# Kernel tuning notes

Measured on AMD Instinct MI355X. Metric: run time of the kernel, lower is better.

Reference implementation:

```python
import jax, jax.numpy as jnp
import numpy as np

B, T, E, V = 4096, 200, 64, 100000
A1, A2 = 64, 32        # attention MLP dims
M1, M2 = 256, 128      # final MLP dims


def setup_inputs() -> dict:
    key = jax.random.key(0)
    ks = jax.random.split(key, 16)
    w = lambda k, shp: (jax.random.normal(k, shp, dtype=jnp.float32) * 0.02)
    return {
        "target_item": jax.random.randint(ks[0], (B,), 0, V),
        "hist_item_id": jax.random.randint(ks[1], (B, T), 0, V),
        "hist_item_id_mask": jnp.ones((B, T), dtype=bool),
        "embed_table": w(ks[2], (V, E)),
        # attention MLP: 4E -> A1 -> A2 -> 1
        "aw1": w(ks[3], (4 * E, A1)), "ab1": jnp.zeros((A1,), jnp.float32),
        "aw2": w(ks[4], (A1, A2)),   "ab2": jnp.zeros((A2,), jnp.float32),
        "aow": w(ks[5], (A2, 1)),    "aob": jnp.zeros((1,), jnp.float32),
        # final MLP: 2E -> M1 -> M2 -> 1
        "mw1": w(ks[6], (2 * E, M1)), "mb1": jnp.zeros((M1,), jnp.float32),
        "mw2": w(ks[7], (M1, M2)),    "mb2": jnp.zeros((M2,), jnp.float32),
        "ow": w(ks[8], (M2, 1)),      "ob": jnp.zeros((1,), jnp.float32),
    }


def reference(target_item, hist_item_id, hist_item_id_mask, embed_table,
              aw1, ab1, aw2, ab2, aow, aob, mw1, mb1, mw2, mb2, ow, ob):
    item_emb = embed_table[target_item]          # [B, E]
    hist_emb = embed_table[hist_item_id]         # [B, T, E]
    q = jnp.broadcast_to(item_emb[:, None, :], hist_emb.shape)  # [B, T, E]
    attn_in = jnp.concatenate([hist_emb, q, hist_emb - q, hist_emb * q], axis=-1)  # [B, T, 4E]
    h = jax.nn.relu(jnp.einsum("bti,ij->btj", attn_in, aw1) + ab1)
    h = jax.nn.relu(jnp.einsum("bti,ij->btj", h, aw2) + ab2)
    scores = (jnp.einsum("bti,io->bto", h, aow) + aob)[..., 0]  # [B, T]
    scores = jnp.where(hist_item_id_mask, scores, -1e9)
    weights = jax.nn.softmax(scores, axis=-1)                   # [B, T]
    interest = jnp.einsum("bt,bte->be", weights, hist_emb)      # [B, E]
    mlp_in = jnp.concatenate([item_emb, interest], axis=-1)     # [B, 2E]
    g = jax.nn.relu(mlp_in @ mw1 + mb1)
    g = jax.nn.relu(g @ mw2 + mb2)
    return g @ ow + ob                                          # [B, 1]
```

## Files before the change

### kernel.cpp

```cpp
#include <hip/hip_runtime.h>
#include <stdint.h>

#define Bq 4096
#define Tq 200
#define TP 208
#define NMT 13
#define Vq 100000
#define BPB 8

typedef __attribute__((ext_vector_type(8))) short short8;
typedef __attribute__((ext_vector_type(4))) float f32x4;
typedef __attribute__((ext_vector_type(4))) unsigned short bfx4;
typedef __attribute__((ext_vector_type(4))) unsigned int u32x4;

static __device__ __forceinline__ unsigned short f2b(float f) {
    unsigned int u = __builtin_bit_cast(unsigned int, f);
    u = u + 0x7fffu + ((u >> 16) & 1u);
    return (unsigned short)(u >> 16);
}
static __device__ __forceinline__ float b2f(unsigned short s) {
    unsigned int u = ((unsigned int)s) << 16;
    return __builtin_bit_cast(float, u);
}
static __device__ __forceinline__ unsigned int pack2(float lo, float hi) {
    unsigned int r;
    asm volatile("v_cvt_pk_bf16_f32 %0, %1, %2" : "=v"(r) : "v"(lo), "v"(hi));
    return r;
}

static __device__ __forceinline__ short8 ld8sw(const unsigned short* base, int row, int col8) {
    return *(const short8*)((const char*)base + (((row << 7) + (col8 << 1)) ^ ((row & 7) << 4)));
}
static __device__ __forceinline__ void st16sw(unsigned short* base, int row, int col, unsigned short v) {
    *(unsigned short*)((char*)base + (((row << 7) + (col << 1)) ^ ((row & 7) << 4))) = v;
}
static __device__ __forceinline__ void st64sw(unsigned short* base, int row, int col4, bfx4 v) {
    *(bfx4*)((char*)base + (((row << 7) + (col4 << 3)) ^ ((row & 7) << 4))) = v;
}
static __device__ __forceinline__ void st128sw(unsigned short* base, int row, int col8, short8 v) {
    *(short8*)((char*)base + (((row << 7) + (col8 << 1)) ^ ((row & 7) << 4))) = v;
}

extern "C" __global__ __launch_bounds__(256) void k_weff(
    const int* __restrict__ target, const float* __restrict__ embed,
    const float* __restrict__ aw1, const float* __restrict__ ab1,
    const float* __restrict__ aw2,
    unsigned short* __restrict__ weff_all, float* __restrict__ qc_all,
    unsigned short* __restrict__ aw2t, unsigned short* __restrict__ embf)
{
    __shared__ float s_C[64][64];
    __shared__ float s_W3[64][64];
    __shared__ float s_W12T[64][65];
    __shared__ float s_qb[BPB][64];
    int tid = threadIdx.x;
    int b0 = blockIdx.x * BPB;

    for (int idx = tid; idx < 4096; idx += 256) {
        int i = idx >> 6, j = idx & 63;
        float a0 = aw1[i * 64 + j];
        float a1 = aw1[(64 + i) * 64 + j];
        float a2 = aw1[(128 + i) * 64 + j];
        float a3 = aw1[(192 + i) * 64 + j];
        s_C[i][j] = a0 + a2;
        s_W3[i][j] = a3;
        s_W12T[j][i] = a1 - a2;
    }
    for (int idx = tid; idx < BPB * 64; idx += 256) {
        int bb = idx >> 6, j = idx & 63;
        s_qb[bb][j] = embed[(long)target[b0 + bb] * 64 + j];
    }
    if (blockIdx.x == 0) {
        for (int idx = tid; idx < 2048; idx += 256) {
            int j = idx >> 5, k = idx & 31;
            aw2t[k * 64 + j] = f2b(aw2[j * 32 + k]);
        }
    }
    __syncthreads();

    for (int p = tid; p < BPB * 64; p += 256) {
        int bb = p >> 6, j = p & 63;
        float acc = ab1[j];
        #pragma unroll 8
        for (int i = 0; i < 64; ++i)
            acc += s_qb[bb][i] * s_W12T[j][i];
        qc_all[(long)(b0 + bb) * 64 + j] = acc;
    }
    int jw = tid >> 2, i0 = (tid & 3) << 4;
    for (int bb = 0; bb < BPB; ++bb) {
        unsigned int pk[8];
        #pragma unroll
        for (int u = 0; u < 8; ++u) {
            int i = i0 + u * 2;
            float w0 = s_C[i][jw] + s_qb[bb][i] * s_W3[i][jw];
            float w1 = s_C[i + 1][jw] + s_qb[bb][i + 1] * s_W3[i + 1][jw];
            pk[u] = pack2(w0, w1);
        }
        u32x4* dst = (u32x4*)(weff_all + (((long)(b0 + bb)) << 12) + jw * 64 + i0);
        u32x4 v0 = { pk[0], pk[1], pk[2], pk[3] };
        u32x4 v1 = { pk[4], pk[5], pk[6], pk[7] };
        dst[0] = v0;
        dst[1] = v1;
    }
    if (embf) {
        long gsz = (long)gridDim.x * 256;
        for (long i = (long)blockIdx.x * 256 + tid; i < (long)Vq * 8; i += gsz) {
            const float* src = embed + i * 8;
            f32x4 e0 = *(const f32x4*)src;
            f32x4 e1 = *(const f32x4*)(src + 4);
            u32x4 pk = { pack2(e0.x, e0.y), pack2(e0.z, e0.w),
                         pack2(e1.x, e1.y), pack2(e1.z, e1.w) };
            *(u32x4*)(embf + i * 8) = pk;
        }
    }
}

extern "C" __global__ __launch_bounds__(256, 4) void k_attn_fast(
    const int* __restrict__ hist, const int* __restrict__ mask,
    const float* __restrict__ embed,
    const float* __restrict__ ab2, const float* __restrict__ aow,
    const float* __restrict__ aob,
    const unsigned short* __restrict__ weff_all,
    const float* __restrict__ qc_all,
    const unsigned short* __restrict__ aw2t,
    const unsigned short* __restrict__ embf,
    float* __restrict__ inter64)
{
    __shared__ alignas(16) unsigned short s_hist[TP * 64];
    __shared__ float s_sc[TP];
    __shared__ float s_red[8];
    __shared__ float s_intp[4][64];

    int tid = threadIdx.x;
    int lane = tid & 63;
    int wv = tid >> 6;
    int b = blockIdx.x;
    int r16 = lane & 15;
    int kg = lane >> 4;

    int tt[7];
    short8 g[7];
    #pragma unroll
    for (int k = 0; k < 7; ++k) {
        int u = tid + k * 256;
        int t = u >> 3;
        if (u < TP * 8) {
            int tc = (t < Tq) ? t : 0;
            int id = hist[b * Tq + tc];
            g[k] = *(const short8*)(embf + (long)id * 64 + (u & 7) * 8);
        }
        tt[k] = t;
    }
    int mk = (tid < Tq) ? mask[(long)b * Tq + tid] : 0;

    short8 wf[4][2];
    #pragma unroll
    for (int n = 0; n < 4; ++n)
        #pragma unroll
        for (int h = 0; h < 2; ++h)
            wf[n][h] = *(const short8*)(weff_all + (((long)b) << 12) + (n * 16 + r16) * 64 + h * 32 + kg * 8);
    short8 af[2][2];
    #pragma unroll
    for (int n = 0; n < 2; ++n)
        #pragma unroll
        for (int h = 0; h < 2; ++h)
            af[n][h] = *(const short8*)(aw2t + (n * 16 + r16) * 64 + h * 32 + kg * 8);
    f32x4 qcv[4];
    #pragma unroll
    for (int n = 0; n < 4; ++n)
        qcv[n] = *(const f32x4*)&qc_all[(long)b * 64 + n * 16 + kg * 4];
    f32x4 ab2v[2], aowv[2];
    #pragma unroll
    for (int n = 0; n < 2; ++n) {
        ab2v[n] = *(const f32x4*)&ab2[n * 16 + kg * 4];
        aowv[n] = *(const f32x4*)&aow[n * 16 + kg * 4];
    }
    float aob0 = aob[0];

    #pragma unroll
    for (int k = 0; k < 7; ++k) {
        int u = tid + k * 256;
        if (u < TP * 8) st128sw(s_hist, tt[k], (u & 7) * 8, g[k]);
    }
    __syncthreads();

    int srcA = r16 + (((kg << 1) & 3) << 4);
    int srcB = srcA + 16;

    for (int m = wv; m < NMT; m += 4) {
        int row0 = m * 16;
        short8 a0 = ld8sw(s_hist, row0 + r16, kg * 8);
        short8 a1 = ld8sw(s_hist, row0 + r16, 32 + kg * 8);
        f32x4 d[4];
        #pragma unroll
        for (int n = 0; n < 4; ++n) {
            f32x4 z = qcv[n];
            z = __builtin_amdgcn_mfma_f32_16x16x32_bf16(wf[n][0], a0, z, 0, 0, 0);
            z = __builtin_amdgcn_mfma_f32_16x16x32_bf16(wf[n][1], a1, z, 0, 0, 0);
            d[n] = z;
        }
        unsigned int p0[4], p1[4];
        #pragma unroll
        for (int n = 0; n < 4; ++n) {
            p0[n] = pack2(fmaxf(d[n][0], 0.f), fmaxf(d[n][1], 0.f));
            p1[n] = pack2(fmaxf(d[n][2], 0.f), fmaxf(d[n][3], 0.f));
        }
        u32x4 w0, w1;
        {
            unsigned int xA0 = __shfl(p0[0], srcA), xA1 = __shfl(p0[1], srcA);
            unsigned int yA0 = __shfl(p1[0], srcA), yA1 = __shfl(p1[1], srcA);
            unsigned int xB0 = __shfl(p0[0], srcB), xB1 = __shfl(p0[1], srcB);
            unsigned int yB0 = __shfl(p1[0], srcB), yB1 = __shfl(p1[1], srcB);
            w0.x = (kg < 2) ? xA0 : xA1;
            w0.y = (kg < 2) ? yA0 : yA1;
            w0.z = (kg < 2) ? xB0 : xB1;
            w0.w = (kg < 2) ? yB0 : yB1;
            unsigned int uA0 = __shfl(p0[2], srcA), uA1 = __shfl(p0[3], srcA);
            unsigned int vA0 = __shfl(p1[2], srcA), vA1 = __shfl(p1[3], srcA);
            unsigned int uB0 = __shfl(p0[2], srcB), uB1 = __shfl(p0[3], srcB);
            unsigned int vB0 = __shfl(p1[2], srcB), vB1 = __shfl(p1[3], srcB);
            w1.x = (kg < 2) ? uA0 : uA1;
            w1.y = (kg < 2) ? vA0 : vA1;
            w1.z = (kg < 2) ? uB0 : uB1;
            w1.w = (kg < 2) ? vB0 : vB1;
        }
        short8 bh0 = __builtin_bit_cast(short8, w0);
        short8 bh1 = __builtin_bit_cast(short8, w1);
        f32x4 e[2];
        #pragma unroll
        for (int n = 0; n < 2; ++n) {
            f32x4 z = { 0.f, 0.f, 0.f, 0.f };
            z = __builtin_amdgcn_mfma_f32_16x16x32_bf16(af[n][0], bh0, z, 0, 0, 0);
            z = __builtin_amdgcn_mfma_f32_16x16x32_bf16(af[n][1], bh1, z, 0, 0, 0);
            e[n] = z;
        }
        float sacc = 0.f;
        #pragma unroll
        for (int n = 0; n < 2; ++n)
            #pragma unroll
            for (int r = 0; r < 4; ++r)
                sacc += fmaxf(e[n][r] + ab2v[n][r], 0.f) * aowv[n][r];
        sacc += __shfl_xor(sacc, 16);
        sacc += __shfl_xor(sacc, 32);
        if (kg == 0) s_sc[row0 + r16] = sacc + aob0;
    }
    __syncthreads();

    float sc = (tid < Tq) ? (mk ? s_sc[tid] : -1e9f) : -1e30f;
    float mx = sc;
    #pragma unroll
    for (int off = 1; off < 64; off <<= 1) mx = fmaxf(mx, __shfl_xor(mx, off));
    if (lane == 0) s_red[wv] = mx;
    __syncthreads();
    mx = fmaxf(fmaxf(s_red[0], s_red[1]), fmaxf(s_red[2], s_red[3]));
    float ex = (tid < Tq) ? expf(sc - mx) : 0.f;
    float sm = ex;
    #pragma unroll
    for (int off = 1; off < 64; off <<= 1) sm += __shfl_xor(sm, off);
    if (lane == 0) s_red[4 + wv] = sm;
    __syncthreads();
    float tot = s_red[4] + s_red[5] + s_red[6] + s_red[7];
    if (tid < Tq) s_sc[tid] = ex / tot;
    else if (tid < TP) s_sc[tid] = 0.f;
    __syncthreads();

    int cg = lane & 7;
    int tg = lane >> 3;
    float acc8[8];
    #pragma unroll
    for (int u = 0; u < 8; ++u) acc8[u] = 0.f;
    for (int t = wv * 8 + tg; t < TP; t += 32) {
        float w = s_sc[t];
        short8 h = ld8sw(s_hist, t, cg * 8);
        #pragma unroll
        for (int u = 0; u < 8; ++u) acc8[u] += w * b2f((unsigned short)h[u]);
    }
    #pragma unroll
    for (int u = 0; u < 8; ++u) {
        acc8[u] += __shfl_xor(acc8[u], 8);
        acc8[u] += __shfl_xor(acc8[u], 16);
        acc8[u] += __shfl_xor(acc8[u], 32);
    }
    if (tg == 0) {
        #pragma unroll
        for (int u = 0; u < 8; ++u) s_intp[wv][cg * 8 + u] = acc8[u];
    }
    __syncthreads();
    if (tid < 64)
        inter64[(long)b * 64 + tid] = s_intp[0][tid] + s_intp[1][tid] + s_intp[2][tid] + s_intp[3][tid];
}

extern "C" __global__ __launch_bounds__(256, 3) void k_attn_fb(
    const int* __restrict__ target, const int* __restrict__ hist,
    const int* __restrict__ mask,
    const float* __restrict__ embed, const float* __restrict__ aw1,
    const float* __restrict__ ab1, const float* __restrict__ aw2,
    const float* __restrict__ ab2, const float* __restrict__ aow,
    const float* __restrict__ aob,
    float* __restrict__ inter64)
{
    __shared__ int s_id[TP];
    __shared__ float s_q[64];
    __shared__ float s_qc[64];
    __shared__ float s_qcp[4][64];
    __shared__ alignas(16) unsigned short s_hist[TP * 64];
    __shared__ alignas(16) unsigned short s_WeffT[64 * 64];
    __shared__ alignas(16) unsigned short s_aw2T[32 * 64];
    __shared__ alignas(16) unsigned short s_h1[4 * 16 * 64];
    __shared__ float s_sc[TP];
    __shared__ float s_aow[32];
    __shared__ float s_ab2[32];
    __shared__ float s_red[8];
    __shared__ float s_intp[4][64];

    int tid = threadIdx.x;
    int lane = tid & 63;
    int wv = tid >> 6;
    int b = blockIdx.x;

    int tgt = target[b];
    if (tid < 64) s_q[tid] = embed[(long)tgt * 64 + tid];
    for (int t = tid; t < TP; t += 256) s_id[t] = hist[b * Tq + ((t < Tq) ? t : 0)];
    if (tid < 32) { s_aow[tid] = aow[tid]; s_ab2[tid] = ab2[tid]; }
    __syncthreads();

    for (int idx = tid; idx < 4096; idx += 256) {
        int i = idx >> 6, j = idx & 63;
        float w = aw1[i * 64 + j] + aw1[(128 + i) * 64 + j] + s_q[i] * aw1[(192 + i) * 64 + j];
        st16sw(s_WeffT, j, i, f2b(w));
    }
    for (int idx = tid; idx < 2048; idx += 256) {
        int j = idx >> 5, k = idx & 31;
        st16sw(s_aw2T, k, j, f2b(aw2[j * 32 + k]));
    }
    {
        float acc = 0.f;
        #pragma unroll
        for (int ii = 0; ii < 16; ++ii) {
            int i = wv * 16 + ii;
            acc += s_q[i] * (aw1[(64 + i) * 64 + lane] - aw1[(128 + i) * 64 + lane]);
        }
        s_qcp[wv][lane] = acc;
    }
    for (int u = tid; u < TP * 16; u += 256) {
        int t = u >> 4, j4 = u & 15;
        f32x4 e = *(const f32x4*)&embed[(long)s_id[t] * 64 + j4 * 4];
        bfx4 p = { f2b(e.x), f2b(e.y), f2b(e.z), f2b(e.w) };
        st64sw(s_hist, t, j4, p);
    }
    __syncthreads();
    if (tid < 64) s_qc[tid] = ab1[tid] + s_qcp[0][tid] + s_qcp[1][tid] + s_qcp[2][tid] + s_qcp[3][tid];
    __syncthreads();

    int r16 = lane & 15;
    int kg = lane >> 4;
    float aob0 = aob[0];
    unsigned short* h1w = s_h1 + wv * 16 * 64;

    for (int m = wv; m < NMT; m += 4) {
        int row0 = m * 16;
        short8 a0 = ld8sw(s_hist, row0 + r16, kg * 8);
        short8 a1 = ld8sw(s_hist, row0 + r16, 32 + kg * 8);
        f32x4 d[4];
        #pragma unroll
        for (int n = 0; n < 4; ++n) {
            short8 b0 = ld8sw(s_WeffT, n * 16 + r16, kg * 8);
            short8 b1 = ld8sw(s_WeffT, n * 16 + r16, 32 + kg * 8);
            float qcv = s_qc[n * 16 + r16];
            f32x4 z = { qcv, qcv, qcv, qcv };
            z = __builtin_amdgcn_mfma_f32_16x16x32_bf16(a0, b0, z, 0, 0, 0);
            z = __builtin_amdgcn_mfma_f32_16x16x32_bf16(a1, b1, z, 0, 0, 0);
            d[n] = z;
        }
        #pragma unroll
        for (int n = 0; n < 4; ++n) {
            int col = n * 16 + r16;
            #pragma unroll
            for (int r = 0; r < 4; ++r)
                st16sw(h1w, kg * 4 + r, col, f2b(fmaxf(d[n][r], 0.f)));
        }
        short8 ha0 = ld8sw(h1w, r16, kg * 8);
        short8 ha1 = ld8sw(h1w, r16, 32 + kg * 8);
        f32x4 e[2];
        #pragma unroll
        for (int n = 0; n < 2; ++n) {
            short8 b0 = ld8sw(s_aw2T, n * 16 + r16, kg * 8);
            short8 b1 = ld8sw(s_aw2T, n * 16 + r16, 32 + kg * 8);
            f32x4 z = { 0.f, 0.f, 0.f, 0.f };
            z = __builtin_amdgcn_mfma_f32_16x16x32_bf16(ha0, b0, z, 0, 0, 0);
            z = __builtin_amdgcn_mfma_f32_16x16x32_bf16(ha1, b1, z, 0, 0, 0);
            e[n] = z;
        }
        #pragma unroll
        for (int r = 0; r < 4; ++r) {
            float h20 = fmaxf(e[0][r] + s_ab2[r16], 0.f);
            float h21 = fmaxf(e[1][r] + s_ab2[16 + r16], 0.f);
            float p = h20 * s_aow[r16] + h21 * s_aow[16 + r16];
            p += __shfl_xor(p, 1);
            p += __shfl_xor(p, 2);
            p += __shfl_xor(p, 4);
            p += __shfl_xor(p, 8);
            if (r16 == 0) s_sc[row0 + kg * 4 + r] = p + aob0;
        }
    }
    __syncthreads();

    float sc = -1e30f;
    if (tid < Tq) {
        int mk = mask[(long)b * Tq + tid];
        sc = mk ? s_sc[tid] : -1e9f;
    }
    float mx = sc;
    #pragma unroll
    for (int off = 1; off < 64; off <<= 1) mx = fmaxf(mx, __shfl_xor(mx, off));
    if (lane == 0) s_red[wv] = mx;
    __syncthreads();
    mx = fmaxf(fmaxf(s_red[0], s_red[1]), fmaxf(s_red[2], s_red[3]));
    float ex = (tid < Tq) ? expf(sc - mx) : 0.f;
    float sm = ex;
    #pragma unroll
    for (int off = 1; off < 64; off <<= 1) sm += __shfl_xor(sm, off);
    if (lane == 0) s_red[4 + wv] = sm;
    __syncthreads();
    float tot = s_red[4] + s_red[5] + s_red[6] + s_red[7];
    if (tid < Tq) s_sc[tid] = ex / tot;
    __syncthreads();

    float acc = 0.f;
    for (int t = wv; t < Tq; t += 4)
        acc += s_sc[t] * b2f(*(const unsigned short*)((const char*)s_hist +
                 (((t << 7) + (lane << 1)) ^ ((t & 7) << 4))));
    s_intp[wv][lane] = acc;
    __syncthreads();
    if (tid < 64)
        inter64[(long)b * 64 + tid] = s_intp[0][tid] + s_intp[1][tid] + s_intp[2][tid] + s_intp[3][tid];
}

extern "C" __global__ __launch_bounds__(256) void k_final(
    const int* __restrict__ target, const float* __restrict__ embed,
    const float* __restrict__ inter64, const float* __restrict__ mw1,
    const float* __restrict__ mb1, const float* __restrict__ mw2,
    const float* __restrict__ mb2, const float* __restrict__ ow,
    const float* __restrict__ ob, float* __restrict__ out)
{
    __shared__ alignas(16) float s_in[8][128];
    __shared__ alignas(16) float s_g1[8][256];
    __shared__ alignas(16) float s_g2[8][128];
    int tid = threadIdx.x;
    long b0 = (long)blockIdx.x * 8;
    for (int idx = tid; idx < 1024; idx += 256) {
        int r = idx >> 7, c = idx & 127;
        s_in[r][c] = (c < 64) ? embed[(long)target[b0 + r] * 64 + c]
                              : inter64[(b0 + r) * 64 + (c - 64)];
    }
    __syncthreads();
    {
        float acc[8];
        float bias = mb1[tid];
        #pragma unroll
        for (int r = 0; r < 8; ++r) acc[r] = bias;
        for (int i0 = 0; i0 < 128; i0 += 4) {
            float w0 = mw1[(i0 + 0) * 256 + tid];
            float w1 = mw1[(i0 + 1) * 256 + tid];
            float w2 = mw1[(i0 + 2) * 256 + tid];
            float w3 = mw1[(i0 + 3) * 256 + tid];
            #pragma unroll
            for (int r = 0; r < 8; ++r) {
                f32x4 e = *(const f32x4*)&s_in[r][i0];
                acc[r] += e.x * w0 + e.y * w1 + e.z * w2 + e.w * w3;
            }
        }
        #pragma unroll
        for (int r = 0; r < 8; ++r) s_g1[r][tid] = fmaxf(acc[r], 0.f);
    }
    __syncthreads();
    {
        int o = tid & 127, rh = tid >> 7;
        float acc[4];
        float bias = mb2[o];
        #pragma unroll
        for (int r = 0; r < 4; ++r) acc[r] = bias;
        for (int i0 = 0; i0 < 256; i0 += 4) {
            float w0 = mw2[(i0 + 0) * 128 + o];
            float w1 = mw2[(i0 + 1) * 128 + o];
            float w2 = mw2[(i0 + 2) * 128 + o];
            float w3 = mw2[(i0 + 3) * 128 + o];
            #pragma unroll
            for (int r = 0; r < 4; ++r) {
                f32x4 e = *(const f32x4*)&s_g1[rh * 4 + r][i0];
                acc[r] += e.x * w0 + e.y * w1 + e.z * w2 + e.w * w3;
            }
        }
        #pragma unroll
        for (int r = 0; r < 4; ++r) s_g2[rh * 4 + r][o] = fmaxf(acc[r], 0.f);
    }
    __syncthreads();
    {
        int r = tid >> 5, l32 = tid & 31;
        float acc = 0.f;
        #pragma unroll
        for (int k = 0; k < 4; ++k) acc += s_g2[r][l32 + k * 32] * ow[l32 + k * 32];
        acc += __shfl_xor(acc, 1);
        acc += __shfl_xor(acc, 2);
        acc += __shfl_xor(acc, 4);
        acc += __shfl_xor(acc, 8);
        acc += __shfl_xor(acc, 16);
        if (l32 == 0) out[b0 + r] = acc + ob[0];
    }
}

extern "C" void kernel_launch(void* const* d_in, const int* in_sizes, int n_in,
                              void* d_out, int out_size, void* d_ws, size_t ws_size,
                              hipStream_t stream)
{
    const int*   target = (const int*)d_in[0];
    const int*   hist   = (const int*)d_in[1];
    const int*   mask   = (const int*)d_in[2];
    const float* embed  = (const float*)d_in[3];
    const float* aw1    = (const float*)d_in[4];
    const float* ab1    = (const float*)d_in[5];
    const float* aw2    = (const float*)d_in[6];
    const float* ab2    = (const float*)d_in[7];
    const float* aow    = (const float*)d_in[8];
    const float* aob    = (const float*)d_in[9];
    const float* mw1    = (const float*)d_in[10];
    const float* mb1    = (const float*)d_in[11];
    const float* mw2    = (const float*)d_in[12];
    const float* mb2    = (const float*)d_in[13];
    const float* ow     = (const float*)d_in[14];
    const float* ob     = (const float*)d_in[15];
    float* out = (float*)d_out;

    const size_t WEFF_B = (size_t)Bq * 4096 * 2;
    const size_t QC_B   = (size_t)Bq * 64 * 4;
    const size_t AW2T_B = 4096;
    const size_t EMBF_B = (size_t)Vq * 64 * 2;
    const size_t INT_B  = (size_t)Bq * 64 * 4;
    char* p = (char*)d_ws;

    if (ws_size >= WEFF_B + QC_B + AW2T_B + EMBF_B + INT_B) {
        unsigned short* weff  = (unsigned short*)p;
        float*          qc    = (float*)(p + WEFF_B);
        unsigned short* aw2t  = (unsigned short*)(p + WEFF_B + QC_B);
        unsigned short* embf  = (unsigned short*)(p + WEFF_B + QC_B + AW2T_B);
        float*          inter = (float*)(p + WEFF_B + QC_B + AW2T_B + EMBF_B);
        k_weff<<<Bq / BPB, 256, 0, stream>>>(target, embed, aw1, ab1, aw2, weff, qc, aw2t, embf);
        k_attn_fast<<<Bq, 256, 0, stream>>>(hist, mask, embed, ab2, aow, aob,
                                            weff, qc, aw2t, embf, inter);
        k_final<<<Bq / 8, 256, 0, stream>>>(target, embed, inter, mw1, mb1, mw2,
                                            mb2, ow, ob, out);
    } else {
        float* inter = (float*)p;
        k_attn_fb<<<Bq, 256, 0, stream>>>(target, hist, mask, embed, aw1, ab1,
                                          aw2, ab2, aow, aob, inter);
        k_final<<<Bq / 8, 256, 0, stream>>>(target, embed, inter, mw1, mb1, mw2,
                                            mb2, ow, ob, out);
    }
}
```

Measured before the change: 92.42 us.

## Compute per-sample effective attention weights inside attention kernel instead of materializing

Removes the 32 MB per-sample bf16 effective-weight buffer that k_weff wrote and k_attn_fast read back. k_weff now stores one shared transposed copy of (W0+W2) and W3 in fp32, produced by block 0. Each attention block loads that copy plus its target embedding and forms the bf16 effective weights in registers. This trades a large global write and read for a few extra FMAs and cached loads of a small shared buffer in every block.

```diff
diff --git a/kernel.cpp b/kernel.cpp
--- a/kernel.cpp
+++ b/kernel.cpp
@@ -45,11 +45,9 @@
     const int* __restrict__ target, const float* __restrict__ embed,
     const float* __restrict__ aw1, const float* __restrict__ ab1,
     const float* __restrict__ aw2,
-    unsigned short* __restrict__ weff_all, float* __restrict__ qc_all,
-    unsigned short* __restrict__ aw2t, unsigned short* __restrict__ embf)
+    float* __restrict__ qc_all, unsigned short* __restrict__ aw2t,
+    float* __restrict__ cw3t, unsigned short* __restrict__ embf)
 {
-    __shared__ float s_C[64][64];
-    __shared__ float s_W3[64][64];
     __shared__ float s_W12T[64][65];
     __shared__ float s_qb[BPB][64];
     int tid = threadIdx.x;
@@ -57,13 +55,7 @@
 
     for (int idx = tid; idx < 4096; idx += 256) {
         int i = idx >> 6, j = idx & 63;
-        float a0 = aw1[i * 64 + j];
-        float a1 = aw1[(64 + i) * 64 + j];
-        float a2 = aw1[(128 + i) * 64 + j];
-        float a3 = aw1[(192 + i) * 64 + j];
-        s_C[i][j] = a0 + a2;
-        s_W3[i][j] = a3;
-        s_W12T[j][i] = a1 - a2;
+        s_W12T[j][i] = aw1[(64 + i) * 64 + j] - aw1[(128 + i) * 64 + j];
     }
     for (int idx = tid; idx < BPB * 64; idx += 256) {
         int bb = idx >> 6, j = idx & 63;
@@ -73,6 +65,11 @@
         for (int idx = tid; idx < 2048; idx += 256) {
             int j = idx >> 5, k = idx & 31;
             aw2t[k * 64 + j] = f2b(aw2[j * 32 + k]);
+        }
+        for (int idx = tid; idx < 4096; idx += 256) {
+            int j = idx >> 6, i = idx & 63;
+            cw3t[j * 64 + i] = aw1[i * 64 + j] + aw1[(128 + i) * 64 + j];
+            cw3t[4096 + j * 64 + i] = aw1[(192 + i) * 64 + j];
         }
     }
     __syncthreads();
@@ -84,22 +81,6 @@
         for (int i = 0; i < 64; ++i)
             acc += s_qb[bb][i] * s_W12T[j][i];
         qc_all[(long)(b0 + bb) * 64 + j] = acc;
-    }
-    int jw = tid >> 2, i0 = (tid & 3) << 4;
-    for (int bb = 0; bb < BPB; ++bb) {
-        unsigned int pk[8];
-        #pragma unroll
-        for (int u = 0; u < 8; ++u) {
-            int i = i0 + u * 2;
-            float w0 = s_C[i][jw] + s_qb[bb][i] * s_W3[i][jw];
-            float w1 = s_C[i + 1][jw] + s_qb[bb][i + 1] * s_W3[i + 1][jw];
-            pk[u] = pack2(w0, w1);
-        }
-        u32x4* dst = (u32x4*)(weff_all + (((long)(b0 + bb)) << 12) + jw * 64 + i0);
-        u32x4 v0 = { pk[0], pk[1], pk[2], pk[3] };
-        u32x4 v1 = { pk[4], pk[5], pk[6], pk[7] };
-        dst[0] = v0;
-        dst[1] = v1;
     }
     if (embf) {
         long gsz = (long)gridDim.x * 256;
@@ -115,13 +96,13 @@
 }
 
 extern "C" __global__ __launch_bounds__(256, 4) void k_attn_fast(
-    const int* __restrict__ hist, const int* __restrict__ mask,
-    const float* __restrict__ embed,
+    const int* __restrict__ target, const int* __restrict__ hist,
+    const int* __restrict__ mask, const float* __restrict__ embed,
     const float* __restrict__ ab2, const float* __restrict__ aow,
     const float* __restrict__ aob,
-    const unsigned short* __restrict__ weff_all,
     const float* __restrict__ qc_all,
     const unsigned short* __restrict__ aw2t,
+    const float* __restrict__ cw3t,
     const unsigned short* __restrict__ embf,
     float* __restrict__ inter64)
 {
@@ -152,12 +133,32 @@
     }
     int mk = (tid < Tq) ? mask[(long)b * Tq + tid] : 0;
 
+    int tgt = target[b];
+    f32x4 qv[2][2];
+    #pragma unroll
+    for (int h = 0; h < 2; ++h) {
+        qv[h][0] = *(const f32x4*)&embed[(long)tgt * 64 + h * 32 + kg * 8];
+        qv[h][1] = *(const f32x4*)&embed[(long)tgt * 64 + h * 32 + kg * 8 + 4];
+    }
     short8 wf[4][2];
     #pragma unroll
-    for (int n = 0; n < 4; ++n)
-        #pragma unroll
-        for (int h = 0; h < 2; ++h)
-            wf[n][h] = *(const short8*)(weff_all + (((long)b) << 12) + (n * 16 + r16) * 64 + h * 32 + kg * 8);
+    for (int n = 0; n < 4; ++n) {
+        int j = n * 16 + r16;
+        #pragma unroll
+        for (int h = 0; h < 2; ++h) {
+            const float* cb = cw3t + j * 64 + h * 32 + kg * 8;
+            f32x4 c0 = *(const f32x4*)cb;
+            f32x4 c1 = *(const f32x4*)(cb + 4);
+            f32x4 w0 = *(const f32x4*)(cb + 4096);
+            f32x4 w1 = *(const f32x4*)(cb + 4100);
+            u32x4 pk;
+            pk.x = pack2(c0.x + qv[h][0].x * w0.x, c0.y + qv[h][0].y * w0.y);
+            pk.y = pack2(c0.z + qv[h][0].z * w0.z, c0.w + qv[h][0].w * w0.w);
+            pk.z = pack2(c1.x + qv[h][1].x * w1.x, c1.y + qv[h][1].y * w1.y);
+            pk.w = pack2(c1.z + qv[h][1].z * w1.z, c1.w + qv[h][1].w * w1.w);
+            wf[n][h] = __builtin_bit_cast(short8, pk);
+        }
+    }
     short8 af[2][2];
     #pragma unroll
     for (int n = 0; n < 2; ++n)
@@ -530,22 +531,22 @@
     const float* ob     = (const float*)d_in[15];
     float* out = (float*)d_out;
 
-    const size_t WEFF_B = (size_t)Bq * 4096 * 2;
     const size_t QC_B   = (size_t)Bq * 64 * 4;
     const size_t AW2T_B = 4096;
+    const size_t CW3T_B = 2 * 4096 * 4;
     const size_t EMBF_B = (size_t)Vq * 64 * 2;
     const size_t INT_B  = (size_t)Bq * 64 * 4;
     char* p = (char*)d_ws;
 
-    if (ws_size >= WEFF_B + QC_B + AW2T_B + EMBF_B + INT_B) {
-        unsigned short* weff  = (unsigned short*)p;
-        float*          qc    = (float*)(p + WEFF_B);
-        unsigned short* aw2t  = (unsigned short*)(p + WEFF_B + QC_B);
-        unsigned short* embf  = (unsigned short*)(p + WEFF_B + QC_B + AW2T_B);
-        float*          inter = (float*)(p + WEFF_B + QC_B + AW2T_B + EMBF_B);
-        k_weff<<<Bq / BPB, 256, 0, stream>>>(target, embed, aw1, ab1, aw2, weff, qc, aw2t, embf);
-        k_attn_fast<<<Bq, 256, 0, stream>>>(hist, mask, embed, ab2, aow, aob,
-                                            weff, qc, aw2t, embf, inter);
+    if (ws_size >= QC_B + AW2T_B + CW3T_B + EMBF_B + INT_B) {
+        float*          qc    = (float*)p;
+        unsigned short* aw2t  = (unsigned short*)(p + QC_B);
+        float*          cw3t  = (float*)(p + QC_B + AW2T_B);
+        unsigned short* embf  = (unsigned short*)(p + QC_B + AW2T_B + CW3T_B);
+        float*          inter = (float*)(p + QC_B + AW2T_B + CW3T_B + EMBF_B);
+        k_weff<<<Bq / BPB, 256, 0, stream>>>(target, embed, aw1, ab1, aw2, qc, aw2t, cw3t, embf);
+        k_attn_fast<<<Bq, 256, 0, stream>>>(target, hist, mask, embed, ab2, aow, aob,
+                                            qc, aw2t, cw3t, embf, inter);
         k_final<<<Bq / 8, 256, 0, stream>>>(target, embed, inter, mw1, mb1, mw2,
                                             mb2, ow, ob, out);
     } else {
```

After: 126.7 us. 1.37x slower.

## Process two batch rows per attention block with prefetch of second row's gathers

Applied to the files above, without the earlier changes.

The attention kernel now handles two batch rows per block. While the first row's scores and softmax run, it issues the embedding gathers, Weff fragments and qc loads for the second row, so the gather latency overlaps compute. It also halves BPB in the weight-precompute kernel, doubling that kernel's grid. The trade-off is higher register pressure from holding the second row's gathered data, which could cut occupancy under the 4-blocks launch bound, and half as many blocks in the attention kernel.

```diff
diff --git a/kernel.cpp b/kernel.cpp
--- a/kernel.cpp
+++ b/kernel.cpp
@@ -6,7 +6,7 @@
 #define TP 208
 #define NMT 13
 #define Vq 100000
-#define BPB 8
+#define BPB 4
 
 typedef __attribute__((ext_vector_type(8))) short short8;
 typedef __attribute__((ext_vector_type(4))) float f32x4;
@@ -113,6 +113,109 @@
         }
     }
 }
+
+#define SCORES_BLOCK(WF, QCV)                                                   \
+    for (int m = wv; m < NMT; m += 4) {                                         \
+        int row0 = m * 16;                                                      \
+        short8 a0 = ld8sw(s_hist, row0 + r16, kg * 8);                          \
+        short8 a1 = ld8sw(s_hist, row0 + r16, 32 + kg * 8);                     \
+        f32x4 d[4];                                                             \
+        _Pragma("unroll")                                                       \
+        for (int n = 0; n < 4; ++n) {                                           \
+            f32x4 z = QCV[n];                                                   \
+            z = __builtin_amdgcn_mfma_f32_16x16x32_bf16(WF[n][0], a0, z, 0, 0, 0); \
+            z = __builtin_amdgcn_mfma_f32_16x16x32_bf16(WF[n][1], a1, z, 0, 0, 0); \
+            d[n] = z;                                                           \
+        }                                                                       \
+        unsigned int p0[4], p1[4];                                              \
+        _Pragma("unroll")                                                       \
+        for (int n = 0; n < 4; ++n) {                                           \
+            p0[n] = pack2(fmaxf(d[n][0], 0.f), fmaxf(d[n][1], 0.f));            \
+            p1[n] = pack2(fmaxf(d[n][2], 0.f), fmaxf(d[n][3], 0.f));            \
+        }                                                                       \
+        u32x4 w0, w1;                                                           \
+        {                                                                       \
+            unsigned int xA0 = __shfl(p0[0], srcA), xA1 = __shfl(p0[1], srcA);  \
+            unsigned int yA0 = __shfl(p1[0], srcA), yA1 = __shfl(p1[1], srcA);  \
+            unsigned int xB0 = __shfl(p0[0], srcB), xB1 = __shfl(p0[1], srcB);  \
+            unsigned int yB0 = __shfl(p1[0], srcB), yB1 = __shfl(p1[1], srcB);  \
+            w0.x = (kg < 2) ? xA0 : xA1;                                        \
+            w0.y = (kg < 2) ? yA0 : yA1;                                        \
+            w0.z = (kg < 2) ? xB0 : xB1;                                        \
+            w0.w = (kg < 2) ? yB0 : yB1;                                        \
+            unsigned int uA0 = __shfl(p0[2], srcA), uA1 = __shfl(p0[3], srcA);  \
+            unsigned int vA0 = __shfl(p1[2], srcA), vA1 = __shfl(p1[3], srcA);  \
+            unsigned int uB0 = __shfl(p0[2], srcB), uB1 = __shfl(p0[3], srcB);  \
+            unsigned int vB0 = __shfl(p1[2], srcB), vB1 = __shfl(p1[3], srcB);  \
+            w1.x = (kg < 2) ? uA0 : uA1;                                        \
+            w1.y = (kg < 2) ? vA0 : vA1;                                        \
+            w1.z = (kg < 2) ? uB0 : uB1;                                        \
+            w1.w = (kg < 2) ? vB0 : vB1;                                        \
+        }                                                                       \
+        short8 bh0 = __builtin_bit_cast(short8, w0);                            \
+        short8 bh1 = __builtin_bit_cast(short8, w1);                            \
+        f32x4 e[2];                                                             \
+        _Pragma("unroll")                                                       \
+        for (int n = 0; n < 2; ++n) {                                           \
+            f32x4 z = { 0.f, 0.f, 0.f, 0.f };                                   \
+            z = __builtin_amdgcn_mfma_f32_16x16x32_bf16(af[n][0], bh0, z, 0, 0, 0); \
+            z = __builtin_amdgcn_mfma_f32_16x16x32_bf16(af[n][1], bh1, z, 0, 0, 0); \
+            e[n] = z;                                                           \
+        }                                                                       \
+        float sacc = 0.f;                                                       \
+        _Pragma("unroll")                                                       \
+        for (int n = 0; n < 2; ++n)                                             \
+            _Pragma("unroll")                                                   \
+            for (int r = 0; r < 4; ++r)                                         \
+                sacc += fmaxf(e[n][r] + ab2v[n][r], 0.f) * aowv[n][r];          \
+        sacc += __shfl_xor(sacc, 16);                                           \
+        sacc += __shfl_xor(sacc, 32);                                           \
+        if (kg == 0) s_sc[row0 + r16] = sacc + aob0;                            \
+    }
+
+#define SOFTMAX_INTEREST_BLOCK(MK, BOUT)                                        \
+    {                                                                           \
+        float sc = (tid < Tq) ? ((MK) ? s_sc[tid] : -1e9f) : -1e30f;            \
+        float mx = sc;                                                          \
+        _Pragma("unroll")                                                       \
+        for (int off = 1; off < 64; off <<= 1) mx = fmaxf(mx, __shfl_xor(mx, off)); \
+        if (lane == 0) s_red[wv] = mx;                                          \
+        __syncthreads();                                                        \
+        mx = fmaxf(fmaxf(s_red[0], s_red[1]), fmaxf(s_red[2], s_red[3]));       \
+        float ex = (tid < Tq) ? expf(sc - mx) : 0.f;                            \
+        float sm = ex;                                                          \
+        _Pragma("unroll")                                                       \
+        for (int off = 1; off < 64; off <<= 1) sm += __shfl_xor(sm, off);       \
+        if (lane == 0) s_red[4 + wv] = sm;                                      \
+        __syncthreads();                                                        \
+        float tot = s_red[4] + s_red[5] + s_red[6] + s_red[7];                  \
+        if (tid < Tq) s_sc[tid] = ex / tot;                                     \
+        else if (tid < TP) s_sc[tid] = 0.f;                                     \
+        __syncthreads();                                                        \
+        float acc8[8];                                                          \
+        _Pragma("unroll")                                                       \
+        for (int u = 0; u < 8; ++u) acc8[u] = 0.f;                              \
+        for (int t = wv * 8 + tg; t < TP; t += 32) {                            \
+            float w = s_sc[t];                                                  \
+            short8 h = ld8sw(s_hist, t, cg * 8);                                \
+            _Pragma("unroll")                                                   \
+            for (int u = 0; u < 8; ++u) acc8[u] += w * b2f((unsigned short)h[u]); \
+        }                                                                       \
+        _Pragma("unroll")                                                       \
+        for (int u = 0; u < 8; ++u) {                                           \
+            acc8[u] += __shfl_xor(acc8[u], 8);                                  \
+            acc8[u] += __shfl_xor(acc8[u], 16);                                 \
+            acc8[u] += __shfl_xor(acc8[u], 32);                                 \
+        }                                                                       \
+        if (tg == 0) {                                                          \
+            _Pragma("unroll")                                                   \
+            for (int u = 0; u < 8; ++u) s_intp[wv][cg * 8 + u] = acc8[u];       \
+        }                                                                       \
+        __syncthreads();                                                        \
+        if (tid < 64)                                                           \
+            inter64[(long)(BOUT) * 64 + tid] =                                  \
+                s_intp[0][tid] + s_intp[1][tid] + s_intp[2][tid] + s_intp[3][tid]; \
+    }
 
 extern "C" __global__ __launch_bounds__(256, 4) void k_attn_fast(
     const int* __restrict__ hist, const int* __restrict__ mask,
@@ -133,9 +236,12 @@
     int tid = threadIdx.x;
     int lane = tid & 63;
     int wv = tid >> 6;
-    int b = blockIdx.x;
     int r16 = lane & 15;
     int kg = lane >> 4;
+    int cg = lane & 7;
+    int tg = lane >> 3;
+    int b0 = blockIdx.x * 2;
+    int b1 = b0 + 1;
 
     int tt[7];
     short8 g[7];
@@ -145,29 +251,37 @@
         int t = u >> 3;
         if (u < TP * 8) {
             int tc = (t < Tq) ? t : 0;
-            int id = hist[b * Tq + tc];
+            int id = hist[b0 * Tq + tc];
             g[k] = *(const short8*)(embf + (long)id * 64 + (u & 7) * 8);
         }
         tt[k] = t;
     }
-    int mk = (tid < Tq) ? mask[(long)b * Tq + tid] : 0;
-
-    short8 wf[4][2];
+    int id1[7];
+    #pragma unroll
+    for (int k = 0; k < 7; ++k) {
+        int u = tid + k * 256;
+        int t = u >> 3;
+        id1[k] = (u < TP * 8) ? hist[b1 * Tq + ((t < Tq) ? t : 0)] : 0;
+    }
+    int mk0 = (tid < Tq) ? mask[(long)b0 * Tq + tid] : 0;
+    int mk1 = (tid < Tq) ? mask[(long)b1 * Tq + tid] : 0;
+
+    short8 wf0[4][2];
     #pragma unroll
     for (int n = 0; n < 4; ++n)
         #pragma unroll
         for (int h = 0; h < 2; ++h)
-            wf[n][h] = *(const short8*)(weff_all + (((long)b) << 12) + (n * 16 + r16) * 64 + h * 32 + kg * 8);
+            wf0[n][h] = *(const short8*)(weff_all + (((long)b0) << 12) + (n * 16 + r16) * 64 + h * 32 + kg * 8);
     short8 af[2][2];
     #pragma unroll
     for (int n = 0; n < 2; ++n)
         #pragma unroll
         for (int h = 0; h < 2; ++h)
             af[n][h] = *(const short8*)(aw2t + (n * 16 + r16) * 64 + h * 32 + kg * 8);
-    f32x4 qcv[4];
+    f32x4 qcv0[4];
     #pragma unroll
     for (int n = 0; n < 4; ++n)
-        qcv[n] = *(const f32x4*)&qc_all[(long)b * 64 + n * 16 + kg * 4];
+        qcv0[n] = *(const f32x4*)&qc_all[(long)b0 * 64 + n * 16 + kg * 4];
     f32x4 ab2v[2], aowv[2];
     #pragma unroll
     for (int n = 0; n < 2; ++n) {
@@ -186,107 +300,39 @@
     int srcA = r16 + (((kg << 1) & 3) << 4);
     int srcB = srcA + 16;
 
-    for (int m = wv; m < NMT; m += 4) {
-        int row0 = m * 16;
-        short8 a0 = ld8sw(s_hist, row0 + r16, kg * 8);
-        short8 a1 = ld8sw(s_hist, row0 + r16, 32 + kg * 8);
-        f32x4 d[4];
-        #pragma unroll
-        for (int n = 0; n < 4; ++n) {
-            f32x4 z = qcv[n];
-            z = __builtin_amdgcn_mfma_f32_16x16x32_bf16(wf[n][0], a0, z, 0, 0, 0);
-            z = __builtin_amdgcn_mfma_f32_16x16x32_bf16(wf[n][1], a1, z, 0, 0, 0);
-            d[n] = z;
-        }
-        unsigned int p0[4], p1[4];
-        #pragma unroll
-        for (int n = 0; n < 4; ++n) {
-            p0[n] = pack2(fmaxf(d[n][0], 0.f), fmaxf(d[n][1], 0.f));
-            p1[n] = pack2(fmaxf(d[n][2], 0.f), fmaxf(d[n][3], 0.f));
-        }
-        u32x4 w0, w1;
-        {
-            unsigned int xA0 = __shfl(p0[0], srcA), xA1 = __shfl(p0[1], srcA);
-            unsigned int yA0 = __shfl(p1[0], srcA), yA1 = __shfl(p1[1], srcA);
-            unsigned int xB0 = __shfl(p0[0], srcB), xB1 = __shfl(p0[1], srcB);
-            unsigned int yB0 = __shfl(p1[0], srcB), yB1 = __shfl(p1[1], srcB);
-            w0.x = (kg < 2) ? xA0 : xA1;
-            w0.y = (kg < 2) ? yA0 : yA1;
-            w0.z = (kg < 2) ? xB0 : xB1;
-            w0.w = (kg < 2) ? yB0 : yB1;
-            unsigned int uA0 = __shfl(p0[2], srcA), uA1 = __shfl(p0[3], srcA);
-            unsigned int vA0 = __shfl(p1[2], srcA), vA1 = __shfl(p1[3], srcA);
-            unsigned int uB0 = __shfl(p0[2], srcB), uB1 = __shfl(p0[3], srcB);
-            unsigned int vB0 = __shfl(p1[2], srcB), vB1 = __shfl(p1[3], srcB);
-            w1.x = (kg < 2) ? uA0 : uA1;
-            w1.y = (kg < 2) ? vA0 : vA1;
-            w1.z = (kg < 2) ? uB0 : uB1;
-            w1.w = (kg < 2) ? vB0 : vB1;
-        }
-        short8 bh0 = __builtin_bit_cast(short8, w0);
-        short8 bh1 = __builtin_bit_cast(short8, w1);
-        f32x4 e[2];
-        #pragma unroll
-        for (int n = 0; n < 2; ++n) {
-            f32x4 z = { 0.f, 0.f, 0.f, 0.f };
-            z = __builtin_amdgcn_mfma_f32_16x16x32_bf16(af[n][0], bh0, z, 0, 0, 0);
-            z = __builtin_amdgcn_mfma_f32_16x16x32_bf16(af[n][1], bh1, z, 0, 0, 0);
-            e[n] = z;
-        }
-        float sacc = 0.f;
-        #pragma unroll
-        for (int n = 0; n < 2; ++n)
-            #pragma unroll
-            for (int r = 0; r < 4; ++r)
-                sacc += fmaxf(e[n][r] + ab2v[n][r], 0.f) * aowv[n][r];
-        sacc += __shfl_xor(sacc, 16);
-        sacc += __shfl_xor(sacc, 32);
-        if (kg == 0) s_sc[row0 + r16] = sacc + aob0;
-    }
-    __syncthreads();
-
-    float sc = (tid < Tq) ? (mk ? s_sc[tid] : -1e9f) : -1e30f;
-    float mx = sc;
-    #pragma unroll
-    for (int off = 1; off < 64; off <<= 1) mx = fmaxf(mx, __shfl_xor(mx, off));
-    if (lane == 0) s_red[wv] = mx;
-    __syncthreads();
-    mx = fmaxf(fmaxf(s_red[0], s_red[1]), fmaxf(s_red[2], s_red[3]));
-    float ex = (tid < Tq) ? expf(sc - mx) : 0.f;
-    float sm = ex;
-    #pragma unroll
-    for (int off = 1; off < 64; off <<= 1) sm += __shfl_xor(sm, off);
-    if (lane == 0) s_red[4 + wv] = sm;
-    __syncthreads();
-    float tot = s_red[4] + s_red[5] + s_red[6] + s_red[7];
-    if (tid < Tq) s_sc[tid] = ex / tot;
-    else if (tid < TP) s_sc[tid] = 0.f;
-    __syncthreads();
-
-    int cg = lane & 7;
-    int tg = lane >> 3;
-    float acc8[8];
-    #pragma unroll
-    for (int u = 0; u < 8; ++u) acc8[u] = 0.f;
-    for (int t = wv * 8 + tg; t < TP; t += 32) {
-        float w = s_sc[t];
-        short8 h = ld8sw(s_hist, t, cg * 8);
-        #pragma unroll
-        for (int u = 0; u < 8; ++u) acc8[u] += w * b2f((unsigned short)h[u]);
-    }
-    #pragma unroll
-    for (int u = 0; u < 8; ++u) {
-        acc8[u] += __shfl_xor(acc8[u], 8);
-        acc8[u] += __shfl_xor(acc8[u], 16);
-        acc8[u] += __shfl_xor(acc8[u], 32);
-    }
-    if (tg == 0) {
-        #pragma unroll
-        for (int u = 0; u < 8; ++u) s_intp[wv][cg * 8 + u] = acc8[u];
-    }
-    __syncthreads();
-    if (tid < 64)
-        inter64[(long)b * 64 + tid] = s_intp[0][tid] + s_intp[1][tid] + s_intp[2][tid] + s_intp[3][tid];
+    SCORES_BLOCK(wf0, qcv0)
+    __syncthreads();
+
+    short8 g1[7];
+    #pragma unroll
+    for (int k = 0; k < 7; ++k) {
+        int u = tid + k * 256;
+        if (u < TP * 8)
+            g1[k] = *(const short8*)(embf + (long)id1[k] * 64 + (u & 7) * 8);
+    }
+    short8 wf1[4][2];
+    #pragma unroll
+    for (int n = 0; n < 4; ++n)
+        #pragma unroll
+        for (int h = 0; h < 2; ++h)
+            wf1[n][h] = *(const short8*)(weff_all + (((long)b1) << 12) + (n * 16 + r16) * 64 + h * 32 + kg * 8);
+    f32x4 qcv1[4];
+    #pragma unroll
+    for (int n = 0; n < 4; ++n)
+        qcv1[n] = *(const f32x4*)&qc_all[(long)b1 * 64 + n * 16 + kg * 4];
+
+    SOFTMAX_INTEREST_BLOCK(mk0, b0)
+    #pragma unroll
+    for (int k = 0; k < 7; ++k) {
+        int u = tid + k * 256;
+        if (u < TP * 8) st128sw(s_hist, tt[k], (u & 7) * 8, g1[k]);
+    }
+    __syncthreads();
+
+    SCORES_BLOCK(wf1, qcv1)
+    __syncthreads();
+
+    SOFTMAX_INTEREST_BLOCK(mk1, b1)
 }
 
 extern "C" __global__ __launch_bounds__(256, 3) void k_attn_fb(
@@ -544,8 +590,8 @@
         unsigned short* embf  = (unsigned short*)(p + WEFF_B + QC_B + AW2T_B);
         float*          inter = (float*)(p + WEFF_B + QC_B + AW2T_B + EMBF_B);
         k_weff<<<Bq / BPB, 256, 0, stream>>>(target, embed, aw1, ab1, aw2, weff, qc, aw2t, embf);
-        k_attn_fast<<<Bq, 256, 0, stream>>>(hist, mask, embed, ab2, aow, aob,
-                                            weff, qc, aw2t, embf, inter);
+        k_attn_fast<<<Bq / 2, 256, 0, stream>>>(hist, mask, embed, ab2, aow, aob,
+                                                weff, qc, aw2t, embf, inter);
         k_final<<<Bq / 8, 256, 0, stream>>>(target, embed, inter, mw1, mb1, mw2,
                                             mb2, ow, ob, out);
     } else {
```

Result: slower. 117.1 us (+26.8%).
